# Kernel optimization log

Hardware: AMD Instinct MI355X
Metric: run time of the kernel (lower is better)

Reference implementation:

```python
import jax, jax.numpy as jnp
import numpy as np

I, H, FC = 118, 1024, 16

def gru_cell(x, h, Wih, Whh, bih, bhh):
    # torch GRU gate order: r, z, n
    gi = x @ Wih.T + bih          # [B, 3H]
    gh = h @ Whh.T + bhh          # [B, 3H]
    i_r, i_z, i_n = jnp.split(gi, 3, axis=-1)
    h_r, h_z, h_n = jnp.split(gh, 3, axis=-1)
    r = jax.nn.sigmoid(i_r + h_r)
    z = jax.nn.sigmoid(i_z + h_z)
    n = jnp.tanh(i_n + r * h_n)
    return (1.0 - z) * n + z * h

def _param(key, shape, fan):
    bound = 1.0 / np.sqrt(fan)
    return jax.random.uniform(key, shape, jnp.float32, -bound, bound)

def setup_inputs() -> dict:
    key = jax.random.key(0)
    ks = jax.random.split(key, 24)
    B, T = 64, 512
    inp = {"x": jax.random.normal(ks[0], (B, T, I), jnp.float32)}
    # encoder 2-layer GRU
    inp["e_Wih0"] = _param(ks[1], (3 * H, I), H); inp["e_Whh0"] = _param(ks[2], (3 * H, H), H)
    inp["e_bih0"] = _param(ks[3], (3 * H,), H);   inp["e_bhh0"] = _param(ks[4], (3 * H,), H)
    inp["e_Wih1"] = _param(ks[5], (3 * H, H), H); inp["e_Whh1"] = _param(ks[6], (3 * H, H), H)
    inp["e_bih1"] = _param(ks[7], (3 * H,), H);   inp["e_bhh1"] = _param(ks[8], (3 * H,), H)
    # decoder 2-layer GRU
    inp["d_Wih0"] = _param(ks[9], (3 * H, I), H);  inp["d_Whh0"] = _param(ks[10], (3 * H, H), H)
    inp["d_bih0"] = _param(ks[11], (3 * H,), H);   inp["d_bhh0"] = _param(ks[12], (3 * H,), H)
    inp["d_Wih1"] = _param(ks[13], (3 * H, H), H); inp["d_Whh1"] = _param(ks[14], (3 * H, H), H)
    inp["d_bih1"] = _param(ks[15], (3 * H,), H);   inp["d_bhh1"] = _param(ks[16], (3 * H,), H)
    # decoder head
    inp["fc_W"] = _param(ks[17], (FC, H), H);  inp["fc_b"] = _param(ks[18], (FC,), H)
    inp["out_W"] = _param(ks[19], (1, FC), FC); inp["out_b"] = _param(ks[20], (1,), FC)
    return inp

def reference(x, e_Wih0, e_Whh0, e_bih0, e_bhh0, e_Wih1, e_Whh1, e_bih1, e_bhh1,
              d_Wih0, d_Whh0, d_bih0, d_bhh0, d_Wih1, d_Whh1, d_bih1, d_bhh1,
              fc_W, fc_b, out_W, out_b):
    B = x.shape[0]
    h1 = jnp.zeros((B, H), x.dtype)
    h2 = jnp.zeros((B, H), x.dtype)

    def enc_step(carry, xt):
        h1, h2 = carry
        h1 = gru_cell(xt, h1, e_Wih0, e_Whh0, e_bih0, e_bhh0)
        h2 = gru_cell(h1, h2, e_Wih1, e_Whh1, e_bih1, e_bhh1)
        return (h1, h2), None

    (h1, h2), _ = jax.lax.scan(enc_step, (h1, h2), jnp.swapaxes(x, 0, 1))  # scan over T

    # decoder: single step (target_length == 1)
    dec_in = x[:, -1, :]                                  # [B, I]
    h1 = gru_cell(dec_in, h1, d_Wih0, d_Whh0, d_bih0, d_bhh0)
    h2 = gru_cell(h1, h2, d_Wih1, d_Whh1, d_bih1, d_bhh1)
    y = jax.nn.relu(h2 @ fc_W.T + fc_b)                   # [B, FC]
    y = y @ out_W.T + out_b                               # [B, 1]
    return y
```

## Files before the change

kernel.cpp:

```cpp
#include <hip/hip_runtime.h>
#include <hip/hip_bf16.h>

#define H_DIM 1024
#define B_DIM 64
#define T_DIM 512
#define I_PAD 128
#define I_ORIG 118
#define FC_DIM 16
#define HB (B_DIM * H_DIM)

typedef __hip_bfloat16 bf16;
typedef __attribute__((ext_vector_type(8))) short short8v;
typedef __attribute__((ext_vector_type(4))) float f32x4;

#define MFMA16(a, b, c) __builtin_amdgcn_mfma_f32_16x16x32_bf16(a, b, c, 0, 0, 0)

__device__ __forceinline__ short8v ldg8(const bf16* p) {
    return *reinterpret_cast<const short8v*>(p);
}
__device__ __forceinline__ short8v ld_byp16(const bf16* p) {
    union { unsigned long long u[2]; short8v v; } r;
    const unsigned long long* q = reinterpret_cast<const unsigned long long*>(p);
    r.u[0] = __hip_atomic_load(q,     __ATOMIC_RELAXED, __HIP_MEMORY_SCOPE_AGENT);
    r.u[1] = __hip_atomic_load(q + 1, __ATOMIC_RELAXED, __HIP_MEMORY_SCOPE_AGENT);
    return r.v;
}
__device__ __forceinline__ unsigned short f2bf_bits(float f) {
    union { bf16 h; unsigned short s; } u;
    u.h = __float2bfloat16(f);
    return u.s;
}
__device__ __forceinline__ unsigned ld_coh(const unsigned* p) {
    return __hip_atomic_load(p, __ATOMIC_RELAXED, __HIP_MEMORY_SCOPE_AGENT);
}
__device__ __forceinline__ void st_coh(unsigned* p, unsigned v) {
    __hip_atomic_store(p, v, __ATOMIC_RELAXED, __HIP_MEMORY_SCOPE_AGENT);
}

__global__ __launch_bounds__(256) void cvt_x_kernel(
    const float* __restrict__ x, bf16* __restrict__ out)
{
    int idx  = blockIdx.x * 256 + threadIdx.x;
    int c    = idx & 127;
    int rest = idx >> 7;
    int b    = rest & 63;
    int t    = rest >> 6;
    float v  = (c < I_ORIG) ? x[((long)b * T_DIM + t) * I_ORIG + c] : 0.0f;
    out[idx] = __float2bfloat16(v);
}

__global__ __launch_bounds__(256) void cvt_pad(
    const float* __restrict__ in, bf16* __restrict__ out,
    int kin, int kp, long total)
{
    long idx = (long)blockIdx.x * 256 + threadIdx.x;
    if (idx >= total) return;
    int  c = (int)(idx % kp);
    long r = idx / kp;
    out[idx] = __float2bfloat16(c < kin ? in[r * kin + c] : 0.0f);
}

__global__ __launch_bounds__(256, 2) void gru_enc2(
    const bf16* __restrict__ x_bf,
    const bf16* __restrict__ Wx1, const bf16* __restrict__ Wh1,
    const bf16* __restrict__ Wx2, const bf16* __restrict__ Wh2,
    const float* __restrict__ bih1, const float* __restrict__ bhh1,
    const float* __restrict__ bih2, const float* __restrict__ bhh2,
    bf16* h1all,
    bf16* h2rg,
    float* hf1f, float* hf2f,
    unsigned* fl)
{
    __shared__ float sm_red[2 * 4608];

    const int tid  = threadIdx.x;
    const int w    = tid >> 6;
    const int lane = tid & 63;
    const int ln   = lane & 15;
    const int lk   = lane >> 4;
    const int bid  = blockIdx.x;
    const int lyr  = bid >> 8;
    const int b2   = bid & 255;
    const int bn   = b2 & 63;
    const int grp  = b2 >> 6;
    const int j0   = bn << 4;
    const int m0   = grp << 4;
    const int j    = j0 + ln;

    const int wko  = w << 8;
    const int crow = (w << 2) | lk;
    const int gm   = m0 + crow;
    const long opos = (long)gm * H_DIM + j;

    const bf16* WhG = lyr ? Wh2 : Wh1;
    short8v whr[8], whz[8], whn[8];
    {
        const bf16* bp = WhG + (long)j * 1024 + wko + lk * 8;
#pragma unroll
        for (int ks = 0; ks < 8; ++ks) {
            whr[ks] = ldg8(bp + ks * 32);
            whz[ks] = ldg8(bp + (1 << 20) + ks * 32);
            whn[ks] = ldg8(bp + (2 << 20) + ks * 32);
        }
    }
    short8v wx_r{}, wx_z{}, wx_n{};
    if (lyr == 0) {
        const bf16* bx = Wx1 + (long)j * I_PAD + (w << 5) + lk * 8;
        wx_r = ldg8(bx);
        wx_z = ldg8(bx + (1 << 17));
        wx_n = ldg8(bx + (2 << 17));
    }

    const float* bihv = lyr ? bih2 : bih1;
    const float* bhhv = lyr ? bhh2 : bhh1;
    const float b_r  = bihv[j] + bhhv[j];
    const float b_z  = bihv[j + 1024] + bhhv[j + 1024];
    const float b_ni = bihv[j + 2048];
    const float b_nh = bhhv[j + 2048];

    unsigned* flbase = fl + (lyr << 10);
    unsigned* myflag = flbase + (grp << 8) + (bn << 2) + w;
    const unsigned* pollp  = flbase + (grp << 8) + (w << 6) + lane;
    const unsigned* pollp1 = fl + (grp << 8) + (w << 6) + lane;

    float hprev = 0.0f;

    if (lyr == 0) {
        short8v xcur;
        {
            const bf16* xr = x_bf + (long)(m0 + ln) * I_PAD + (w << 5) + lk * 8;
            xcur = ldg8(xr);
        }
        for (int t = 0; t < T_DIM; ++t) {
            f32x4 aR{0,0,0,0}, aZ{0,0,0,0}, aNI{0,0,0,0}, aNH{0,0,0,0};

            aR  = MFMA16(xcur, wx_r, aR);
            aZ  = MFMA16(xcur, wx_z, aZ);
            aNI = MFMA16(xcur, wx_n, aNI);

            if (t > 0) {
                const unsigned tgt = (unsigned)t;
                while (true) {
                    unsigned fv = ld_coh(pollp);
                    if (__all((int)(fv >= tgt))) break;
                }
                asm volatile("" ::: "memory");
            }

            const bf16* ha = h1all + (long)t * HB + (long)(m0 + ln) * H_DIM
                             + wko + lk * 8;
            short8v ah[8];
#pragma unroll
            for (int ks = 0; ks < 8; ++ks) ah[ks] = ldg8(ha + ks * 32);
#pragma unroll
            for (int ks = 0; ks < 8; ++ks) {
                aR  = MFMA16(ah[ks], whr[ks], aR);
                aZ  = MFMA16(ah[ks], whz[ks], aZ);
                aNH = MFMA16(ah[ks], whn[ks], aNH);
            }

            float* red = sm_red + (t & 1) * 4608;
#pragma unroll
            for (int a = 0; a < 4; ++a) {
                f32x4 v = (a == 0) ? aR : (a == 1) ? aZ : (a == 2) ? aNI : aNH;
                int base = ((w << 2) + a) * 288 + (lk * 4) * 18 + ln;
#pragma unroll
                for (int e = 0; e < 4; ++e) red[base + e * 18] = v[e];
            }
            __syncthreads();

            float sR = 0, sZ = 0, sNI = 0, sNH = 0;
#pragma unroll
            for (int w2 = 0; w2 < 4; ++w2) {
                int tb = (w2 << 2) * 288 + crow * 18 + ln;
                sR  += red[tb];
                sZ  += red[tb + 288];
                sNI += red[tb + 576];
                sNH += red[tb + 864];
            }
            float rr = 1.0f / (1.0f + __expf(-(sR + b_r)));
            float zz = 1.0f / (1.0f + __expf(-(sZ + b_z)));
            float xn = (sNI + b_ni) + rr * (sNH + b_nh);
            float nn = 2.0f / (1.0f + __expf(-2.0f * xn)) - 1.0f;
            float hv = (1.0f - zz) * nn + zz * hprev;
            hprev = hv;

            bf16* dst = h1all + (long)(t + 1) * HB;
            float ho = __shfl_xor(hv, 1);
            if ((ln & 1) == 0) {
                unsigned pk = (unsigned)f2bf_bits(hv)
                            | ((unsigned)f2bf_bits(ho) << 16);
                st_coh((unsigned*)(dst + (opos & ~1L)), pk);
            }
            if (t == T_DIM - 1) hf1f[opos] = hv;

            asm volatile("s_waitcnt vmcnt(0)" ::: "memory");
            if (lane == 0) st_coh(myflag, (unsigned)(t + 1));
            if (t + 1 < T_DIM) {
                const bf16* xr = x_bf + (long)(t + 1) * (B_DIM * I_PAD)
                               + (long)(m0 + ln) * I_PAD + (w << 5) + lk * 8;
                xcur = ldg8(xr);
            }
        }
    } else {
        const bf16* wx2r = Wx2 + (long)j * 1024 + wko + lk * 8;
        for (int t = 0; t < T_DIM; ++t) {
            {
                const unsigned tgt = (unsigned)(t + 1);
                while (true) {
                    unsigned fv = ld_coh(pollp1);
                    if (__all((int)(fv >= tgt))) break;
                }
                asm volatile("" ::: "memory");
            }
            const bf16* xa = h1all + (long)(t + 1) * HB
                             + (long)(m0 + ln) * H_DIM + wko + lk * 8;
            short8v ai[8];
#pragma unroll
            for (int ks = 0; ks < 8; ++ks) ai[ks] = ldg8(xa + ks * 32);

            f32x4 aR{0,0,0,0}, aZ{0,0,0,0}, aNI{0,0,0,0}, aNH{0,0,0,0};
#pragma unroll
            for (int ks = 0; ks < 8; ++ks) {
                short8v br  = ldg8(wx2r + ks * 32);
                short8v bz  = ldg8(wx2r + (1 << 20) + ks * 32);
                short8v bnn = ldg8(wx2r + (2 << 20) + ks * 32);
                aR  = MFMA16(ai[ks], br,  aR);
                aZ  = MFMA16(ai[ks], bz,  aZ);
                aNI = MFMA16(ai[ks], bnn, aNI);
            }

            if (t > 0) {
                const unsigned tgt = (unsigned)t;
                while (true) {
                    unsigned fv = ld_coh(pollp);
                    if (__all((int)(fv >= tgt))) break;
                }
                asm volatile("" ::: "memory");
            }
            const bf16* hb = h2rg + (long)((t + 3) & 3) * HB
                             + (long)(m0 + ln) * H_DIM + wko + lk * 8;
            short8v ah[8];
#pragma unroll
            for (int ks = 0; ks < 8; ++ks) ah[ks] = ld_byp16(hb + ks * 32);
#pragma unroll
            for (int ks = 0; ks < 8; ++ks) {
                aR  = MFMA16(ah[ks], whr[ks], aR);
                aZ  = MFMA16(ah[ks], whz[ks], aZ);
                aNH = MFMA16(ah[ks], whn[ks], aNH);
            }

            float* red = sm_red + (t & 1) * 4608;
#pragma unroll
            for (int a = 0; a < 4; ++a) {
                f32x4 v = (a == 0) ? aR : (a == 1) ? aZ : (a == 2) ? aNI : aNH;
                int base = ((w << 2) + a) * 288 + (lk * 4) * 18 + ln;
#pragma unroll
                for (int e = 0; e < 4; ++e) red[base + e * 18] = v[e];
            }
            __syncthreads();

            float sR = 0, sZ = 0, sNI = 0, sNH = 0;
#pragma unroll
            for (int w2 = 0; w2 < 4; ++w2) {
                int tb = (w2 << 2) * 288 + crow * 18 + ln;
                sR  += red[tb];
                sZ  += red[tb + 288];
                sNI += red[tb + 576];
                sNH += red[tb + 864];
            }
            float rr = 1.0f / (1.0f + __expf(-(sR + b_r)));
            float zz = 1.0f / (1.0f + __expf(-(sZ + b_z)));
            float xn = (sNI + b_ni) + rr * (sNH + b_nh);
            float nn = 2.0f / (1.0f + __expf(-2.0f * xn)) - 1.0f;
            float hv = (1.0f - zz) * nn + zz * hprev;
            hprev = hv;

            bf16* dst = h2rg + (long)(t & 3) * HB;
            float ho = __shfl_xor(hv, 1);
            if ((ln & 1) == 0) {
                unsigned pk = (unsigned)f2bf_bits(hv)
                            | ((unsigned)f2bf_bits(ho) << 16);
                st_coh((unsigned*)(dst + (opos & ~1L)), pk);
            }
            if (t == T_DIM - 1) hf2f[opos] = hv;

            if (t + 1 < T_DIM) {
                asm volatile("s_waitcnt vmcnt(0)" ::: "memory");
                if (lane == 0) st_coh(myflag, (unsigned)(t + 1));
            }
        }
    }
}

template<int WXK, bool WXG, bool SEQ>
__global__ __launch_bounds__(256, 1) void gru_pass(
    const bf16* __restrict__ xbase, long xstride,
    const bf16* __restrict__ WxG,
    const bf16* __restrict__ WhG,
    const float* __restrict__ bih, const float* __restrict__ bhh,
    const bf16* hin, bf16* hout,
    const float* f_init, float* f_final,
    int nsteps, unsigned* flags)
{
    extern __shared__ char smem[];
    constexpr int WH_BYTES = 3 * 16 * 1024 * 2;
    constexpr int WX_BYTES = WXG ? 0 : 3 * 16 * WXK * 2;
    float* sm_red = (float*)(smem + WH_BYTES + WX_BYTES);

    const int tid  = threadIdx.x;
    const int w    = tid >> 6;
    const int lane = tid & 63;
    const int ln   = lane & 15;
    const int lk   = lane >> 4;
    const int bid  = blockIdx.x;
    const int bn   = bid & 63;
    const int grp  = bid >> 6;
    const int j0   = bn * 16;
    const int m0   = grp * 16;
    const int j    = j0 + ln;

    for (int c = tid; c < WH_BYTES / 16; c += 256) {
        int lin = c * 16;
        int row = lin >> 11;
        int wb  = lin & 2047;
        int g   = row >> 4, jj = row & 15;
        const bf16* src = WhG + ((long)(g * 1024 + j0 + jj) << 10) + (wb >> 1);
        *reinterpret_cast<short8v*>(smem + (lin ^ ((jj & 7) << 4))) = ldg8(src);
    }
    if constexpr (!WXG) {
        for (int c = tid; c < WX_BYTES / 16; c += 256) {
            int lin = c * 16;
            int row = lin / (WXK * 2);
            int wb  = lin % (WXK * 2);
            int g   = row >> 4, jj = row & 15;
            const bf16* src = WxG + (long)(g * 1024 + j0 + jj) * WXK + (wb >> 1);
            *reinterpret_cast<short8v*>(smem + WH_BYTES + (lin ^ ((jj & 7) << 4))) = ldg8(src);
        }
    }
    __syncthreads();

    const int wkoh = w << 8;
    const int wkox = (WXK == 128) ? (w << 5) : (w << 8);
    const int swz  = (ln & 7) << 4;
    const int whb0 = ln * 2048 + ((wkoh + lk * 8) << 1);

    const float bias_r  = bih[j] + bhh[j];
    const float bias_z  = bih[j + H_DIM] + bhh[j + H_DIM];
    const float bias_ni = bih[j + 2 * H_DIM];
    const float bias_nh = bhh[j + 2 * H_DIM];

    const int  crow = (w << 2) | lk;
    const int  gm   = m0 + crow;
    const long opos = (long)gm * H_DIM + j;

    float hprev = f_init ? f_init[opos] : 0.0f;

    constexpr int NKX = (WXK == 128) ? 1 : 8;
    short8v xcur[NKX];
    {
        const bf16* xr = xbase + (long)(m0 + ln) * WXK + wkox + lk * 8;
#pragma unroll
        for (int ks = 0; ks < NKX; ++ks) xcur[ks] = ldg8(xr + ks * 32);
    }

    for (int t = 0; t < nsteps; ++t) {
        f32x4 aR{0,0,0,0}, aZ{0,0,0,0}, aNI{0,0,0,0}, aNH{0,0,0,0};

        if constexpr (WXK == 128) {
            int o = WH_BYTES + ln * 256 + ((wkox + lk * 8) << 1);
            short8v br  = *(const short8v*)(smem + ((o       ) ^ swz));
            short8v bz  = *(const short8v*)(smem + ((o + 4096) ^ swz));
            short8v bnn = *(const short8v*)(smem + ((o + 8192) ^ swz));
            aR  = MFMA16(xcur[0], br,  aR);
            aZ  = MFMA16(xcur[0], bz,  aZ);
            aNI = MFMA16(xcur[0], bnn, aNI);
        } else {
            const bf16* wxr = WxG + (long)(j0 + ln) * 1024 + wkox + lk * 8;
#pragma unroll
            for (int ks = 0; ks < 8; ++ks) {
                short8v br  = ldg8(wxr + ks * 32);
                short8v bz  = ldg8(wxr + (1 << 20) + ks * 32);
                short8v bnn = ldg8(wxr + (2 << 20) + ks * 32);
                aR  = MFMA16(xcur[ks], br,  aR);
                aZ  = MFMA16(xcur[ks], bz,  aZ);
                aNI = MFMA16(xcur[ks], bnn, aNI);
            }
        }

        const bf16* bf_in = SEQ ? hin + (long)t * HB : hin + (long)(t & 1) * HB;
        const bf16* ha = bf_in + (long)(m0 + ln) * H_DIM + wkoh + lk * 8;
        short8v ah[8];
#pragma unroll
        for (int ks = 0; ks < 8; ++ks)
            ah[ks] = SEQ ? ldg8(ha + ks * 32) : ld_byp16(ha + ks * 32);

#pragma unroll
        for (int ks = 0; ks < 8; ++ks) {
            int o = whb0 + ks * 64;
            short8v br  = *(const short8v*)(smem + ((o        ) ^ swz));
            short8v bz  = *(const short8v*)(smem + ((o + 32768) ^ swz));
            short8v bnn = *(const short8v*)(smem + ((o + 65536) ^ swz));
            aR  = MFMA16(ah[ks], br,  aR);
            aZ  = MFMA16(ah[ks], bz,  aZ);
            aNH = MFMA16(ah[ks], bnn, aNH);
        }

        float* red = sm_red + (t & 1) * 4608;
#pragma unroll
        for (int a = 0; a < 4; ++a) {
            f32x4 v = (a == 0) ? aR : (a == 1) ? aZ : (a == 2) ? aNI : aNH;
            int base = ((w << 2) + a) * 288 + (lk * 4) * 18 + ln;
#pragma unroll
            for (int e = 0; e < 4; ++e)
                red[base + e * 18] = v[e];
        }
        __syncthreads();

        float sR = 0, sZ = 0, sNI = 0, sNH = 0;
#pragma unroll
        for (int w2 = 0; w2 < 4; ++w2) {
            int tb = (w2 << 2) * 288 + crow * 18 + ln;
            sR  += red[tb];
            sZ  += red[tb + 288];
            sNI += red[tb + 576];
            sNH += red[tb + 864];
        }
        float rr = 1.0f / (1.0f + __expf(-(sR + bias_r)));
        float zz = 1.0f / (1.0f + __expf(-(sZ + bias_z)));
        float xn = (sNI + bias_ni) + rr * (sNH + bias_nh);
        float nn = 2.0f / (1.0f + __expf(-2.0f * xn)) - 1.0f;
        float hv = (1.0f - zz) * nn + zz * hprev;
        hprev = hv;

        {
            bf16* wr = SEQ ? hout + (long)t * HB
                           : const_cast<bf16*>(hin) + (long)((t + 1) & 1) * HB;
            float ho = __shfl_xor(hv, 1);
            if ((ln & 1) == 0) {
                unsigned pk = (unsigned)f2bf_bits(hv)
                            | ((unsigned)f2bf_bits(ho) << 16);
                st_coh((unsigned*)(wr + (opos & ~1L)), pk);
            }
        }
        if (t == nsteps - 1 && f_final) f_final[opos] = hv;
        (void)flags;
    }
}

__global__ __launch_bounds__(1024) void head_kernel(
    const float* __restrict__ h2,
    const float* __restrict__ fc_W, const float* __restrict__ fc_b,
    const float* __restrict__ out_W, const float* __restrict__ out_b,
    float* __restrict__ y)
{
    __shared__ float acc_s[FC_DIM][B_DIM];
    const int b = threadIdx.x & 63;
    const int f = threadIdx.x >> 6;
    const float* wp = fc_W + (long)f * H_DIM;
    const float* hp = h2 + (long)b * H_DIM;
    float a = fc_b[f];
#pragma unroll 8
    for (int k = 0; k < H_DIM; ++k)
        a = fmaf(hp[k], wp[k], a);
    a = fmaxf(a, 0.0f);
    acc_s[f][b] = a * out_W[f];
    __syncthreads();
    if (threadIdx.x < 64) {
        float s = out_b[0];
#pragma unroll
        for (int f2 = 0; f2 < FC_DIM; ++f2) s += acc_s[f2][b];
        y[b] = s;
    }
}

extern "C" void kernel_launch(void* const* d_in, const int* in_sizes, int n_in,
                              void* d_out, int out_size, void* d_ws, size_t ws_size,
                              hipStream_t stream)
{
    const float* x      = (const float*)d_in[0];
    const float* e_Wih0 = (const float*)d_in[1];
    const float* e_Whh0 = (const float*)d_in[2];
    const float* e_bih0 = (const float*)d_in[3];
    const float* e_bhh0 = (const float*)d_in[4];
    const float* e_Wih1 = (const float*)d_in[5];
    const float* e_Whh1 = (const float*)d_in[6];
    const float* e_bih1 = (const float*)d_in[7];
    const float* e_bhh1 = (const float*)d_in[8];
    const float* d_Wih0 = (const float*)d_in[9];
    const float* d_Whh0 = (const float*)d_in[10];
    const float* d_bih0 = (const float*)d_in[11];
    const float* d_bhh0 = (const float*)d_in[12];
    const float* d_Wih1 = (const float*)d_in[13];
    const float* d_Whh1 = (const float*)d_in[14];
    const float* d_bih1 = (const float*)d_in[15];
    const float* d_bhh1 = (const float*)d_in[16];
    const float* fc_W   = (const float*)d_in[17];
    const float* fc_b   = (const float*)d_in[18];
    const float* out_W  = (const float*)d_in[19];
    const float* out_b  = (const float*)d_in[20];
    (void)in_sizes; (void)n_in; (void)out_size; (void)ws_size;

    char* p = (char*)d_ws;
    auto alloc = [&](size_t bytes) -> char* {
        char* r = p; p += (bytes + 255) & ~(size_t)255; return r;
    };
    bf16*  x_bf  = (bf16*)alloc((size_t)T_DIM * B_DIM * I_PAD * 2);
    bf16*  wih0e = (bf16*)alloc(3072ull * 128 * 2);
    bf16*  whh0e = (bf16*)alloc(3072ull * 1024 * 2);
    bf16*  wih1e = (bf16*)alloc(3072ull * 1024 * 2);
    bf16*  whh1e = (bf16*)alloc(3072ull * 1024 * 2);
    bf16*  wih0d = (bf16*)alloc(3072ull * 128 * 2);
    bf16*  whh0d = (bf16*)alloc(3072ull * 1024 * 2);
    bf16*  wih1d = (bf16*)alloc(3072ull * 1024 * 2);
    bf16*  whh1d = (bf16*)alloc(3072ull * 1024 * 2);
    bf16*  h1all = (bf16*)alloc(514ull * HB * 2);
    bf16*  h2rg  = (bf16*)alloc(5ull * HB * 2);
    bf16*  hd1b  = (bf16*)alloc((size_t)HB * 2);
    float* hf1f  = (float*)alloc((size_t)HB * 4);
    float* hf2f  = (float*)alloc((size_t)HB * 4);
    float* hd1f  = (float*)alloc((size_t)HB * 4);
    float* hd2f  = (float*)alloc((size_t)HB * 4);
    unsigned* fl = (unsigned*)alloc(8192);

    constexpr int RED = 2 * 4608 * 4;
    constexpr int S1  = 98304 + 12288 + RED;
    constexpr int S2  = 98304 + RED;
    (void)hipFuncSetAttribute((const void*)gru_pass<128, false, true>,
                              hipFuncAttributeMaxDynamicSharedMemorySize, S1);
    (void)hipFuncSetAttribute((const void*)gru_pass<1024, true, false>,
                              hipFuncAttributeMaxDynamicSharedMemorySize, S2);

    cvt_x_kernel<<<(T_DIM * B_DIM * I_PAD) / 256, 256, 0, stream>>>(x, x_bf);
    auto cvt = [&](const float* in, bf16* out, int kin, int kp) {
        long total = 3072L * kp;
        cvt_pad<<<(int)((total + 255) / 256), 256, 0, stream>>>(in, out, kin, kp, total);
    };
    cvt(e_Wih0, wih0e, 118, 128);
    cvt(e_Whh0, whh0e, 1024, 1024);
    cvt(e_Wih1, wih1e, 1024, 1024);
    cvt(e_Whh1, whh1e, 1024, 1024);
    cvt(d_Wih0, wih0d, 118, 128);
    cvt(d_Whh0, whh0d, 1024, 1024);
    cvt(d_Wih1, wih1d, 1024, 1024);
    cvt(d_Whh1, whh1d, 1024, 1024);

    hipMemsetAsync(h1all, 0, (size_t)HB * 2, stream);
    hipMemsetAsync(h2rg + 3ull * HB, 0, (size_t)HB * 2, stream);
    hipMemsetAsync(fl,    0, 8192, stream);

    gru_enc2<<<512, 256, 0, stream>>>(
        x_bf, wih0e, whh0e, wih1e, whh1e,
        e_bih0, e_bhh0, e_bih1, e_bhh1,
        h1all, h2rg, hf1f, hf2f, fl);

    gru_pass<128, false, true><<<256, 256, S1, stream>>>(
        x_bf + 511L * B_DIM * I_PAD, 0, wih0d, whh0d, d_bih0, d_bhh0,
        h1all + 512L * HB, hd1b, hf1f, hd1f, 1, nullptr);

    gru_pass<1024, true, false><<<256, 256, S2, stream>>>(
        hd1b, 0, wih1d, whh1d, d_bih1, d_bhh1,
        h2rg + 3L * HB, nullptr, hf2f, hd2f, 1, nullptr);

    head_kernel<<<1, 1024, 0, stream>>>(hd2f, fc_W, fc_b, out_W, out_b,
                                        (float*)d_out);
}
```

Measured before the change: 5.056 ms.

## Halve encoder grid by giving each block 32 batch rows

The fused two-layer encoder now launches 256 blocks instead of 512. Each block handles 32 batch rows as two 16-row MFMA tiles that share the register-resident recurrent weights, so weight reuse doubles and fewer blocks take part in the per-step flag barrier. Layer-2 input projections for the next step are computed right after the current step's flag is published, taking them off the critical path. Costs are more registers per block (occupancy hint lowered to 1), larger dynamic shared memory for the reduction, and twice the MFMA and load work per block on the serial chain.

```diff
diff --git a/kernel.cpp b/kernel.cpp
--- a/kernel.cpp
+++ b/kernel.cpp
@@ -60,7 +60,7 @@
     out[idx] = __float2bfloat16(c < kin ? in[r * kin + c] : 0.0f);
 }
 
-__global__ __launch_bounds__(256, 2) void gru_enc2(
+__global__ __launch_bounds__(256, 1) void gru_enc2(
     const bf16* __restrict__ x_bf,
     const bf16* __restrict__ Wx1, const bf16* __restrict__ Wh1,
     const bf16* __restrict__ Wx2, const bf16* __restrict__ Wh2,
@@ -71,7 +71,7 @@
     float* hf1f, float* hf2f,
     unsigned* fl)
 {
-    __shared__ float sm_red[2 * 4608];
+    extern __shared__ float sm_red[];
 
     const int tid  = threadIdx.x;
     const int w    = tid >> 6;
@@ -79,18 +79,18 @@
     const int ln   = lane & 15;
     const int lk   = lane >> 4;
     const int bid  = blockIdx.x;
-    const int lyr  = bid >> 8;
-    const int b2   = bid & 255;
+    const int lyr  = bid >> 7;
+    const int b2   = bid & 127;
     const int bn   = b2 & 63;
     const int grp  = b2 >> 6;
     const int j0   = bn << 4;
-    const int m0   = grp << 4;
+    const int m0   = grp << 5;
     const int j    = j0 + ln;
 
     const int wko  = w << 8;
-    const int crow = (w << 2) | lk;
-    const int gm   = m0 + crow;
-    const long opos = (long)gm * H_DIM + j;
+    const int r0   = (w << 2) | lk;
+    const long opos0 = (long)(m0 + r0) * H_DIM + j;
+    const long opos1 = opos0 + 16L * H_DIM;
 
     const bf16* WhG = lyr ? Wh2 : Wh1;
     short8v whr[8], whz[8], whn[8];
@@ -118,179 +118,205 @@
     const float b_ni = bihv[j + 2048];
     const float b_nh = bhhv[j + 2048];
 
-    unsigned* flbase = fl + (lyr << 10);
+    unsigned* flbase = fl + (lyr << 9);
     unsigned* myflag = flbase + (grp << 8) + (bn << 2) + w;
-    const unsigned* pollp  = flbase + (grp << 8) + (w << 6) + lane;
-    const unsigned* pollp1 = fl + (grp << 8) + (w << 6) + lane;
-
-    float hprev = 0.0f;
+    const unsigned* pollp  = flbase + (grp << 8) + (lane << 2);
+    const unsigned* pollp1 = fl + (grp << 8) + (lane << 2);
+
+    float hprev0 = 0.0f, hprev1 = 0.0f;
+
+#define POLL4(PTR, TGT)                                                      \
+    {                                                                        \
+        const unsigned _t = (TGT);                                           \
+        while (true) {                                                       \
+            unsigned f0 = ld_coh((PTR) + 0), f1 = ld_coh((PTR) + 1);         \
+            unsigned f2 = ld_coh((PTR) + 2), f3 = ld_coh((PTR) + 3);         \
+            int ok = (f0 >= _t) & (f1 >= _t) & (f2 >= _t) & (f3 >= _t);      \
+            if (__all(ok)) break;                                            \
+        }                                                                    \
+        asm volatile("" ::: "memory");                                       \
+    }
+
+#define REDUCE_COMBINE(RED, A_R0, A_Z0, A_NI0, A_NH0, A_R1, A_Z1, A_NI1, A_NH1) \
+    {                                                                        \
+        _Pragma("unroll")                                                    \
+        for (int a = 0; a < 4; ++a) {                                        \
+            f32x4 v0 = (a == 0) ? A_R0 : (a == 1) ? A_Z0 : (a == 2) ? A_NI0 : A_NH0; \
+            f32x4 v1 = (a == 0) ? A_R1 : (a == 1) ? A_Z1 : (a == 2) ? A_NI1 : A_NH1; \
+            int base = ((w << 2) + a) * 576 + (lk << 2) * 18 + ln;           \
+            _Pragma("unroll")                                                \
+            for (int e = 0; e < 4; ++e) {                                    \
+                (RED)[base + e * 18] = v0[e];                                \
+                (RED)[base + 288 + e * 18] = v1[e];                          \
+            }                                                                \
+        }                                                                    \
+        __syncthreads();                                                     \
+        _Pragma("unroll")                                                    \
+        for (int mh = 0; mh < 2; ++mh) {                                     \
+            float sR = 0, sZ = 0, sNI = 0, sNH = 0;                          \
+            _Pragma("unroll")                                                \
+            for (int w2 = 0; w2 < 4; ++w2) {                                 \
+                int tb = (w2 << 2) * 576 + mh * 288 + r0 * 18 + ln;          \
+                sR  += (RED)[tb];                                            \
+                sZ  += (RED)[tb + 576];                                      \
+                sNI += (RED)[tb + 1152];                                     \
+                sNH += (RED)[tb + 1728];                                     \
+            }                                                                \
+            float rr = 1.0f / (1.0f + __expf(-(sR + b_r)));                  \
+            float zz = 1.0f / (1.0f + __expf(-(sZ + b_z)));                  \
+            float xn = (sNI + b_ni) + rr * (sNH + b_nh);                     \
+            float nn = 2.0f / (1.0f + __expf(-2.0f * xn)) - 1.0f;            \
+            float hp = mh ? hprev1 : hprev0;                                 \
+            float hv = (1.0f - zz) * nn + zz * hp;                           \
+            if (mh) { hprev1 = hv; hv1 = hv; } else { hprev0 = hv; hv0 = hv; } \
+        }                                                                    \
+    }
 
     if (lyr == 0) {
-        short8v xcur;
+        short8v xc0, xc1;
         {
             const bf16* xr = x_bf + (long)(m0 + ln) * I_PAD + (w << 5) + lk * 8;
-            xcur = ldg8(xr);
+            xc0 = ldg8(xr);
+            xc1 = ldg8(xr + 16L * I_PAD);
         }
         for (int t = 0; t < T_DIM; ++t) {
-            f32x4 aR{0,0,0,0}, aZ{0,0,0,0}, aNI{0,0,0,0}, aNH{0,0,0,0};
-
-            aR  = MFMA16(xcur, wx_r, aR);
-            aZ  = MFMA16(xcur, wx_z, aZ);
-            aNI = MFMA16(xcur, wx_n, aNI);
-
-            if (t > 0) {
-                const unsigned tgt = (unsigned)t;
-                while (true) {
-                    unsigned fv = ld_coh(pollp);
-                    if (__all((int)(fv >= tgt))) break;
-                }
-                asm volatile("" ::: "memory");
-            }
-
-            const bf16* ha = h1all + (long)t * HB + (long)(m0 + ln) * H_DIM
-                             + wko + lk * 8;
-            short8v ah[8];
-#pragma unroll
-            for (int ks = 0; ks < 8; ++ks) ah[ks] = ldg8(ha + ks * 32);
+            f32x4 aR0{0,0,0,0}, aZ0{0,0,0,0}, aNI0{0,0,0,0}, aNH0{0,0,0,0};
+            f32x4 aR1{0,0,0,0}, aZ1{0,0,0,0}, aNI1{0,0,0,0}, aNH1{0,0,0,0};
+
+            aR0  = MFMA16(xc0, wx_r, aR0);  aR1  = MFMA16(xc1, wx_r, aR1);
+            aZ0  = MFMA16(xc0, wx_z, aZ0);  aZ1  = MFMA16(xc1, wx_z, aZ1);
+            aNI0 = MFMA16(xc0, wx_n, aNI0); aNI1 = MFMA16(xc1, wx_n, aNI1);
+
+            if (t > 0) POLL4(pollp, (unsigned)t);
+
+            const bf16* ha0 = h1all + (long)t * HB + (long)(m0 + ln) * H_DIM
+                              + wko + lk * 8;
+            const bf16* ha1 = ha0 + 16L * H_DIM;
+            short8v ah0[8], ah1[8];
+#pragma unroll
+            for (int ks = 0; ks < 8; ++ks) ah0[ks] = ldg8(ha0 + ks * 32);
+#pragma unroll
+            for (int ks = 0; ks < 8; ++ks) ah1[ks] = ldg8(ha1 + ks * 32);
 #pragma unroll
             for (int ks = 0; ks < 8; ++ks) {
-                aR  = MFMA16(ah[ks], whr[ks], aR);
-                aZ  = MFMA16(ah[ks], whz[ks], aZ);
-                aNH = MFMA16(ah[ks], whn[ks], aNH);
-            }
-
-            float* red = sm_red + (t & 1) * 4608;
-#pragma unroll
-            for (int a = 0; a < 4; ++a) {
-                f32x4 v = (a == 0) ? aR : (a == 1) ? aZ : (a == 2) ? aNI : aNH;
-                int base = ((w << 2) + a) * 288 + (lk * 4) * 18 + ln;
-#pragma unroll
-                for (int e = 0; e < 4; ++e) red[base + e * 18] = v[e];
-            }
-            __syncthreads();
-
-            float sR = 0, sZ = 0, sNI = 0, sNH = 0;
-#pragma unroll
-            for (int w2 = 0; w2 < 4; ++w2) {
-                int tb = (w2 << 2) * 288 + crow * 18 + ln;
-                sR  += red[tb];
-                sZ  += red[tb + 288];
-                sNI += red[tb + 576];
-                sNH += red[tb + 864];
-            }
-            float rr = 1.0f / (1.0f + __expf(-(sR + b_r)));
-            float zz = 1.0f / (1.0f + __expf(-(sZ + b_z)));
-            float xn = (sNI + b_ni) + rr * (sNH + b_nh);
-            float nn = 2.0f / (1.0f + __expf(-2.0f * xn)) - 1.0f;
-            float hv = (1.0f - zz) * nn + zz * hprev;
-            hprev = hv;
+                aR0  = MFMA16(ah0[ks], whr[ks], aR0);
+                aZ0  = MFMA16(ah0[ks], whz[ks], aZ0);
+                aNH0 = MFMA16(ah0[ks], whn[ks], aNH0);
+                aR1  = MFMA16(ah1[ks], whr[ks], aR1);
+                aZ1  = MFMA16(ah1[ks], whz[ks], aZ1);
+                aNH1 = MFMA16(ah1[ks], whn[ks], aNH1);
+            }
+
+            float hv0, hv1;
+            float* red = sm_red + (t & 1) * 9216;
+            REDUCE_COMBINE(red, aR0, aZ0, aNI0, aNH0, aR1, aZ1, aNI1, aNH1);
 
             bf16* dst = h1all + (long)(t + 1) * HB;
-            float ho = __shfl_xor(hv, 1);
+            float ho0 = __shfl_xor(hv0, 1), ho1 = __shfl_xor(hv1, 1);
             if ((ln & 1) == 0) {
-                unsigned pk = (unsigned)f2bf_bits(hv)
-                            | ((unsigned)f2bf_bits(ho) << 16);
-                st_coh((unsigned*)(dst + (opos & ~1L)), pk);
-            }
-            if (t == T_DIM - 1) hf1f[opos] = hv;
+                unsigned p0 = (unsigned)f2bf_bits(hv0) | ((unsigned)f2bf_bits(ho0) << 16);
+                unsigned p1 = (unsigned)f2bf_bits(hv1) | ((unsigned)f2bf_bits(ho1) << 16);
+                st_coh((unsigned*)(dst + (opos0 & ~1L)), p0);
+                st_coh((unsigned*)(dst + (opos1 & ~1L)), p1);
+            }
+            if (t == T_DIM - 1) { hf1f[opos0] = hv0; hf1f[opos1] = hv1; }
 
             asm volatile("s_waitcnt vmcnt(0)" ::: "memory");
             if (lane == 0) st_coh(myflag, (unsigned)(t + 1));
             if (t + 1 < T_DIM) {
                 const bf16* xr = x_bf + (long)(t + 1) * (B_DIM * I_PAD)
                                + (long)(m0 + ln) * I_PAD + (w << 5) + lk * 8;
-                xcur = ldg8(xr);
+                xc0 = ldg8(xr);
+                xc1 = ldg8(xr + 16L * I_PAD);
             }
         }
     } else {
         const bf16* wx2r = Wx2 + (long)j * 1024 + wko + lk * 8;
-        for (int t = 0; t < T_DIM; ++t) {
-            {
-                const unsigned tgt = (unsigned)(t + 1);
-                while (true) {
-                    unsigned fv = ld_coh(pollp1);
-                    if (__all((int)(fv >= tgt))) break;
-                }
-                asm volatile("" ::: "memory");
-            }
-            const bf16* xa = h1all + (long)(t + 1) * HB
-                             + (long)(m0 + ln) * H_DIM + wko + lk * 8;
-            short8v ai[8];
-#pragma unroll
-            for (int ks = 0; ks < 8; ++ks) ai[ks] = ldg8(xa + ks * 32);
-
-            f32x4 aR{0,0,0,0}, aZ{0,0,0,0}, aNI{0,0,0,0}, aNH{0,0,0,0};
+
+        f32x4 gR0{0,0,0,0}, gZ0{0,0,0,0}, gN0{0,0,0,0};
+        f32x4 gR1{0,0,0,0}, gZ1{0,0,0,0}, gN1{0,0,0,0};
+        {
+            POLL4(pollp1, 1u);
+            const bf16* xa0 = h1all + 1L * HB + (long)(m0 + ln) * H_DIM
+                              + wko + lk * 8;
+            const bf16* xa1 = xa0 + 16L * H_DIM;
 #pragma unroll
             for (int ks = 0; ks < 8; ++ks) {
                 short8v br  = ldg8(wx2r + ks * 32);
                 short8v bz  = ldg8(wx2r + (1 << 20) + ks * 32);
                 short8v bnn = ldg8(wx2r + (2 << 20) + ks * 32);
-                aR  = MFMA16(ai[ks], br,  aR);
-                aZ  = MFMA16(ai[ks], bz,  aZ);
-                aNI = MFMA16(ai[ks], bnn, aNI);
-            }
-
-            if (t > 0) {
-                const unsigned tgt = (unsigned)t;
-                while (true) {
-                    unsigned fv = ld_coh(pollp);
-                    if (__all((int)(fv >= tgt))) break;
+                short8v a0  = ldg8(xa0 + ks * 32);
+                short8v a1  = ldg8(xa1 + ks * 32);
+                gR0 = MFMA16(a0, br, gR0);   gR1 = MFMA16(a1, br, gR1);
+                gZ0 = MFMA16(a0, bz, gZ0);   gZ1 = MFMA16(a1, bz, gZ1);
+                gN0 = MFMA16(a0, bnn, gN0);  gN1 = MFMA16(a1, bnn, gN1);
+            }
+        }
+
+        for (int t = 0; t < T_DIM; ++t) {
+            if (t > 0) POLL4(pollp, (unsigned)t);
+
+            f32x4 aR0 = gR0, aZ0 = gZ0, aNI0 = gN0, aNH0{0,0,0,0};
+            f32x4 aR1 = gR1, aZ1 = gZ1, aNI1 = gN1, aNH1{0,0,0,0};
+
+            const bf16* hb0 = h2rg + (long)((t + 3) & 3) * HB
+                              + (long)(m0 + ln) * H_DIM + wko + lk * 8;
+            const bf16* hb1 = hb0 + 16L * H_DIM;
+            short8v ah0[8], ah1[8];
+#pragma unroll
+            for (int ks = 0; ks < 8; ++ks) ah0[ks] = ld_byp16(hb0 + ks * 32);
+#pragma unroll
+            for (int ks = 0; ks < 8; ++ks) ah1[ks] = ld_byp16(hb1 + ks * 32);
+#pragma unroll
+            for (int ks = 0; ks < 8; ++ks) {
+                aR0  = MFMA16(ah0[ks], whr[ks], aR0);
+                aZ0  = MFMA16(ah0[ks], whz[ks], aZ0);
+                aNH0 = MFMA16(ah0[ks], whn[ks], aNH0);
+                aR1  = MFMA16(ah1[ks], whr[ks], aR1);
+                aZ1  = MFMA16(ah1[ks], whz[ks], aZ1);
+                aNH1 = MFMA16(ah1[ks], whn[ks], aNH1);
+            }
+
+            float hv0, hv1;
+            float* red = sm_red + (t & 1) * 9216;
+            REDUCE_COMBINE(red, aR0, aZ0, aNI0, aNH0, aR1, aZ1, aNI1, aNH1);
+
+            bf16* dst = h2rg + (long)(t & 3) * HB;
+            float ho0 = __shfl_xor(hv0, 1), ho1 = __shfl_xor(hv1, 1);
+            if ((ln & 1) == 0) {
+                unsigned p0 = (unsigned)f2bf_bits(hv0) | ((unsigned)f2bf_bits(ho0) << 16);
+                unsigned p1 = (unsigned)f2bf_bits(hv1) | ((unsigned)f2bf_bits(ho1) << 16);
+                st_coh((unsigned*)(dst + (opos0 & ~1L)), p0);
+                st_coh((unsigned*)(dst + (opos1 & ~1L)), p1);
+            }
+            if (t == T_DIM - 1) { hf2f[opos0] = hv0; hf2f[opos1] = hv1; }
+
+            asm volatile("s_waitcnt vmcnt(0)" ::: "memory");
+            if (lane == 0 && t + 1 < T_DIM) st_coh(myflag, (unsigned)(t + 1));
+
+            if (t + 1 < T_DIM) {
+                POLL4(pollp1, (unsigned)(t + 2));
+                const bf16* xa0 = h1all + (long)(t + 2) * HB
+                                  + (long)(m0 + ln) * H_DIM + wko + lk * 8;
+                const bf16* xa1 = xa0 + 16L * H_DIM;
+                gR0 = f32x4{0,0,0,0}; gZ0 = f32x4{0,0,0,0}; gN0 = f32x4{0,0,0,0};
+                gR1 = f32x4{0,0,0,0}; gZ1 = f32x4{0,0,0,0}; gN1 = f32x4{0,0,0,0};
+#pragma unroll
+                for (int ks = 0; ks < 8; ++ks) {
+                    short8v br  = ldg8(wx2r + ks * 32);
+                    short8v bz  = ldg8(wx2r + (1 << 20) + ks * 32);
+                    short8v bnn = ldg8(wx2r + (2 << 20) + ks * 32);
+                    short8v a0  = ldg8(xa0 + ks * 32);
+                    short8v a1  = ldg8(xa1 + ks * 32);
+                    gR0 = MFMA16(a0, br, gR0);   gR1 = MFMA16(a1, br, gR1);
+                    gZ0 = MFMA16(a0, bz, gZ0);   gZ1 = MFMA16(a1, bz, gZ1);
+                    gN0 = MFMA16(a0, bnn, gN0);  gN1 = MFMA16(a1, bnn, gN1);
                 }
-                asm volatile("" ::: "memory");
-            }
-            const bf16* hb = h2rg + (long)((t + 3) & 3) * HB
-                             + (long)(m0 + ln) * H_DIM + wko + lk * 8;
-            short8v ah[8];
-#pragma unroll
-            for (int ks = 0; ks < 8; ++ks) ah[ks] = ld_byp16(hb + ks * 32);
-#pragma unroll
-            for (int ks = 0; ks < 8; ++ks) {
-                aR  = MFMA16(ah[ks], whr[ks], aR);
-                aZ  = MFMA16(ah[ks], whz[ks], aZ);
-                aNH = MFMA16(ah[ks], whn[ks], aNH);
-            }
-
-            float* red = sm_red + (t & 1) * 4608;
-#pragma unroll
-            for (int a = 0; a < 4; ++a) {
-                f32x4 v = (a == 0) ? aR : (a == 1) ? aZ : (a == 2) ? aNI : aNH;
-                int base = ((w << 2) + a) * 288 + (lk * 4) * 18 + ln;
-#pragma unroll
-                for (int e = 0; e < 4; ++e) red[base + e * 18] = v[e];
-            }
-            __syncthreads();
-
-            float sR = 0, sZ = 0, sNI = 0, sNH = 0;
-#pragma unroll
-            for (int w2 = 0; w2 < 4; ++w2) {
-                int tb = (w2 << 2) * 288 + crow * 18 + ln;
-                sR  += red[tb];
-                sZ  += red[tb + 288];
-                sNI += red[tb + 576];
-                sNH += red[tb + 864];
-            }
-            float rr = 1.0f / (1.0f + __expf(-(sR + b_r)));
-            float zz = 1.0f / (1.0f + __expf(-(sZ + b_z)));
-            float xn = (sNI + b_ni) + rr * (sNH + b_nh);
-            float nn = 2.0f / (1.0f + __expf(-2.0f * xn)) - 1.0f;
-            float hv = (1.0f - zz) * nn + zz * hprev;
-            hprev = hv;
-
-            bf16* dst = h2rg + (long)(t & 3) * HB;
-            float ho = __shfl_xor(hv, 1);
-            if ((ln & 1) == 0) {
-                unsigned pk = (unsigned)f2bf_bits(hv)
-                            | ((unsigned)f2bf_bits(ho) << 16);
-                st_coh((unsigned*)(dst + (opos & ~1L)), pk);
-            }
-            if (t == T_DIM - 1) hf2f[opos] = hv;
-
-            if (t + 1 < T_DIM) {
-                asm volatile("s_waitcnt vmcnt(0)" ::: "memory");
-                if (lane == 0) st_coh(myflag, (unsigned)(t + 1));
-            }
-        }
-    }
+            }
+        }
+    }
+#undef POLL4
+#undef REDUCE_COMBINE
 }
 
 template<int WXK, bool WXG, bool SEQ>
@@ -524,8 +550,11 @@
     unsigned* fl = (unsigned*)alloc(8192);
 
     constexpr int RED = 2 * 4608 * 4;
+    constexpr int SE  = 2 * 9216 * 4;
     constexpr int S1  = 98304 + 12288 + RED;
     constexpr int S2  = 98304 + RED;
+    (void)hipFuncSetAttribute((const void*)gru_enc2,
+                              hipFuncAttributeMaxDynamicSharedMemorySize, SE);
     (void)hipFuncSetAttribute((const void*)gru_pass<128, false, true>,
                               hipFuncAttributeMaxDynamicSharedMemorySize, S1);
     (void)hipFuncSetAttribute((const void*)gru_pass<1024, true, false>,
@@ -549,7 +578,7 @@
     hipMemsetAsync(h2rg + 3ull * HB, 0, (size_t)HB * 2, stream);
     hipMemsetAsync(fl,    0, 8192, stream);
 
-    gru_enc2<<<512, 256, 0, stream>>>(
+    gru_enc2<<<256, 256, SE, stream>>>(
         x_bf, wih0e, whh0e, wih1e, whh1e,
         e_bih0, e_bhh0, e_bih1, e_bhh1,
         h1all, h2rg, hf1f, hf2f, fl);
```

Result: slower. 5.822 ms (+15.1%).
